# Performance work log

Hardware: AMD Instinct MI355X
Metric: run time of the kernel (lower is better)

## Reference

```python
import jax, jax.numpy as jnp
import numpy as np

NEG_SLOPE = 0.2
EPS = 1e-16


def glorot(key, shape):
    fan_in, fan_out = shape[0], shape[-1]
    lim = jnp.sqrt(6.0 / (fan_in + fan_out))
    return jax.random.uniform(key, shape, jnp.float32, -lim, lim)


def setup_inputs() -> dict:
    key = jax.random.key(0)
    ks = jax.random.split(key, 20)
    N, E, Fin, C, H = 50000, 800000, 128, 64, 4
    x = jax.random.normal(ks[0], (N, Fin), jnp.float32)
    edge_index = jax.random.randint(ks[1], (2, E), 0, N, jnp.int64)
    edge_attr = jax.random.normal(ks[2], (E, 1), jnp.float32)
    # GATConv layer 1: Fin -> C per head, H heads, concat
    W1 = glorot(ks[3], (Fin, H * C))
    att_src1 = glorot(ks[4], (H, C))
    att_dst1 = glorot(ks[5], (H, C))
    We1 = glorot(ks[6], (1, H * C))
    att_e1 = glorot(ks[7], (H, C))
    b1 = jnp.zeros((H * C,), jnp.float32)
    # GATConv layer 2: H*C -> C, 1 head, no concat
    W2 = glorot(ks[8], (H * C, C))
    att_src2 = glorot(ks[9], (1, C))
    att_dst2 = glorot(ks[10], (1, C))
    We2 = glorot(ks[11], (1, C))
    att_e2 = glorot(ks[12], (1, C))
    b2 = jnp.zeros((C,), jnp.float32)
    # classifier
    Wfc = glorot(ks[13], (C, 2))
    bfc = jnp.zeros((2,), jnp.float32)
    return dict(x=x, edge_index=edge_index, edge_attr=edge_attr,
                W1=W1, att_src1=att_src1, att_dst1=att_dst1, We1=We1, att_e1=att_e1, b1=b1,
                W2=W2, att_src2=att_src2, att_dst2=att_dst2, We2=We2, att_e2=att_e2, b2=b2,
                Wfc=Wfc, bfc=bfc)


def gat_conv(x, src, dst, edge_attr, W, att_src, att_dst, We, att_e, bias, concat):
    N = x.shape[0]
    H, C = att_src.shape
    h = (x @ W).reshape(N, H, C)                       # [N,H,C]
    a_src = jnp.sum(h * att_src, axis=-1)              # [N,H]
    a_dst = jnp.sum(h * att_dst, axis=-1)              # [N,H]
    e = (edge_attr @ We).reshape(-1, H, C)             # [E,H,C]
    a_e = jnp.sum(e * att_e, axis=-1)                  # [E,H]
    alpha = a_src[src] + a_dst[dst] + a_e              # [E,H]
    alpha = jax.nn.leaky_relu(alpha, NEG_SLOPE)
    # segment softmax over destination nodes
    amax = jax.lax.stop_gradient(jax.ops.segment_max(alpha, dst, num_segments=N))
    expa = jnp.exp(alpha - amax[dst])
    denom = jax.ops.segment_sum(expa, dst, num_segments=N)
    alpha = expa / (denom[dst] + EPS)                  # [E,H]
    msg = h[src] * alpha[:, :, None]                   # [E,H,C]
    out = jax.ops.segment_sum(msg, dst, num_segments=N)  # [N,H,C]
    out = out.reshape(N, H * C) if concat else out.mean(axis=1)
    return out + bias


def reference(x, edge_index, edge_attr,
              W1, att_src1, att_dst1, We1, att_e1, b1,
              W2, att_src2, att_dst2, We2, att_e2, b2,
              Wfc, bfc):
    N = x.shape[0]
    # add self loops (PyG GATConv default, fill_value='mean' for edge_attr)
    loop = jnp.arange(N, dtype=edge_index.dtype)
    src = jnp.concatenate([edge_index[0], loop])
    dst = jnp.concatenate([edge_index[1], loop])
    ea_mean = jnp.mean(edge_attr, axis=0, keepdims=True)
    ea = jnp.concatenate([edge_attr, jnp.broadcast_to(ea_mean, (N, edge_attr.shape[1]))])
    h = gat_conv(x, src, dst, ea, W1, att_src1, att_dst1, We1, att_e1, b1, concat=True)
    h = jax.nn.elu(h)
    # dropout: eval mode -> identity
    h = gat_conv(h, src, dst, ea, W2, att_src2, att_dst2, We2, att_e2, b2, concat=False)
    emb = jax.nn.elu(h)
    logits = emb @ Wfc + bfc
    return jax.nn.log_softmax(logits, axis=1), emb
```

## Files before the change

### kernel.cpp

```cpp
#include <hip/hip_runtime.h>
#include <math.h>

#define NEG_SLOPE 0.2f
#define EPSF 1e-16f

constexpr int FIN = 128;
constexpr int H1  = 4;
constexpr int C   = 64;
constexpr int HC  = 256;

typedef __attribute__((ext_vector_type(8))) short bf16x8;
typedef __attribute__((ext_vector_type(4))) float f32x4;

__device__ inline float wredsum(float v) {
#pragma unroll
    for (int off = 32; off; off >>= 1) v += __shfl_down(v, off);
    return v;
}
__device__ inline float wredmax(float v) {
#pragma unroll
    for (int off = 32; off; off >>= 1) v = fmaxf(v, __shfl_down(v, off));
    return v;
}
__device__ inline float4 wredmax4(float4 v) {
#pragma unroll
    for (int off = 32; off; off >>= 1) {
        v.x = fmaxf(v.x, __shfl_down(v.x, off));
        v.y = fmaxf(v.y, __shfl_down(v.y, off));
        v.z = fmaxf(v.z, __shfl_down(v.z, off));
        v.w = fmaxf(v.w, __shfl_down(v.w, off));
    }
    return v;
}
__device__ inline float4 wredsum4(float4 v) {
#pragma unroll
    for (int off = 32; off; off >>= 1) {
        v.x += __shfl_down(v.x, off);
        v.y += __shfl_down(v.y, off);
        v.z += __shfl_down(v.z, off);
        v.w += __shfl_down(v.w, off);
    }
    return v;
}
__device__ inline float4 bcast4(float4 v) {
    v.x = __shfl(v.x, 0); v.y = __shfl(v.y, 0);
    v.z = __shfl(v.z, 0); v.w = __shfl(v.w, 0);
    return v;
}
__device__ inline float comp4(float4 v, int i) {
    return i == 0 ? v.x : (i == 1 ? v.y : (i == 2 ? v.z : v.w));
}
__device__ inline unsigned short f2bf(float f) {
    unsigned u = __float_as_uint(f);
    return (unsigned short)((u + 0x7fffu + ((u >> 16) & 1u)) >> 16);
}

__global__ void k_ea_sum(const float* __restrict__ ea, int E, float* __restrict__ scal) {
    int i = blockIdx.x * blockDim.x + threadIdx.x;
    float v = (i < E) ? ea[i] : 0.0f;
    v = wredsum(v);
    __shared__ float sm[4];
    if ((threadIdx.x & 63) == 0) sm[threadIdx.x >> 6] = v;
    __syncthreads();
    if (threadIdx.x == 0) atomicAdd(scal, sm[0] + sm[1] + sm[2] + sm[3]);
}

__global__ void k_prep(const float* __restrict__ We1, const float* __restrict__ ae1,
                       const float* __restrict__ We2, const float* __restrict__ ae2,
                       float* __restrict__ scal, float inv_E) {
    int t = threadIdx.x;
    float p = We1[t] * ae1[t];
    p = wredsum(p);
    if ((t & 63) == 0) scal[4 + (t >> 6)] = p;
    if (t < 64) {
        float q = We2[t] * ae2[t];
        q = wredsum(q);
        if (t == 0) scal[2] = q;
    }
    if (t == 0) scal[1] = scal[0] * inv_E;
}

__global__ void k_convw(const float* __restrict__ W1, const float* __restrict__ W2,
                        unsigned short* __restrict__ W1f, unsigned short* __restrict__ W2f) {
    int idx = blockIdx.x * 256 + threadIdx.x;
    {
        int j = idx & 7, l = (idx >> 3) & 63, t = (idx >> 9) & 3, q = idx >> 11;
        int k = t * 32 + (l >> 4) * 8 + j;
        int n = 16 * q + (l & 15);
        W1f[idx] = f2bf(W1[k * HC + n]);
    }
    if (idx < 16384) {
        int j = idx & 7, l = (idx >> 3) & 63, t = (idx >> 9) & 7, g = idx >> 12;
        int k = t * 32 + (l >> 4) * 8 + j;
        int c = 16 * g + (l & 15);
        W2f[idx] = f2bf(W2[k * C + c]);
    }
}

__global__ void k_hist(const int* __restrict__ ei, int* __restrict__ deg, int E, int Etot) {
    int e = blockIdx.x * blockDim.x + threadIdx.x;
    if (e >= Etot) return;
    int d = (e < E) ? ei[E + e] : e - E;
    atomicAdd(&deg[d], 1);
}

__global__ void k_scan1(const int* __restrict__ deg, int* __restrict__ rowstart,
                        int* __restrict__ bsums, int N) {
    __shared__ int sm[256];
    int i = blockIdx.x * 256 + threadIdx.x;
    int v = (i < N) ? deg[i] : 0;
    sm[threadIdx.x] = v;
    __syncthreads();
    for (int off = 1; off < 256; off <<= 1) {
        int t = (threadIdx.x >= off) ? sm[threadIdx.x - off] : 0;
        __syncthreads();
        sm[threadIdx.x] += t;
        __syncthreads();
    }
    if (i < N) rowstart[i] = sm[threadIdx.x] - v;
    if (threadIdx.x == 255) bsums[blockIdx.x] = sm[255];
}

__global__ void k_scan2(int* __restrict__ bsums, int nb) {
    __shared__ int sm[256];
    int v = (threadIdx.x < nb) ? bsums[threadIdx.x] : 0;
    sm[threadIdx.x] = v;
    __syncthreads();
    for (int off = 1; off < 256; off <<= 1) {
        int t = (threadIdx.x >= off) ? sm[threadIdx.x - off] : 0;
        __syncthreads();
        sm[threadIdx.x] += t;
        __syncthreads();
    }
    if (threadIdx.x < nb) bsums[threadIdx.x] = sm[threadIdx.x] - v;
}

__global__ void k_scan3(int* __restrict__ rowstart, const int* __restrict__ bsums, int N) {
    int i = blockIdx.x * 256 + threadIdx.x;
    if (i < N) rowstart[i] += bsums[blockIdx.x];
}

__global__ void k_scatter(const int* __restrict__ ei, const float* __restrict__ eattr,
                          const float* __restrict__ scal, const int* __restrict__ rowstart,
                          int* __restrict__ cursor, int2* __restrict__ csr, int E, int Etot) {
    int e = blockIdx.x * blockDim.x + threadIdx.x;
    if (e >= Etot) return;
    int s, d; float ea;
    if (e < E) { s = ei[e]; d = ei[E + e]; ea = eattr[e]; }
    else       { s = e - E; d = s;          ea = scal[1]; }
    int pos = atomicAdd(&cursor[d], 1);
    csr[rowstart[d] + pos] = make_int2(s, __float_as_int(ea));
}

__global__ void k_gemm1(const float* __restrict__ x, const unsigned short* __restrict__ W1f,
                        const float* __restrict__ attsrc, const float* __restrict__ attdst,
                        unsigned short* __restrict__ h1b,
                        float* __restrict__ a_src, float* __restrict__ a_dst) {
    __shared__ unsigned short xs[16 * 128];
    __shared__ unsigned short hs[16 * 256];
    int t = threadIdx.x;
    int n0 = blockIdx.x * 16;
    {
        const float4* xg = (const float4*)(x + (size_t)n0 * FIN);
        float4 v0 = xg[t * 2], v1 = xg[t * 2 + 1];
        int row = t >> 4;
        int ch = (t & 15) ^ (row & 7);
        uint4 p;
        p.x = f2bf(v0.x) | ((unsigned)f2bf(v0.y) << 16);
        p.y = f2bf(v0.z) | ((unsigned)f2bf(v0.w) << 16);
        p.z = f2bf(v1.x) | ((unsigned)f2bf(v1.y) << 16);
        p.w = f2bf(v1.z) | ((unsigned)f2bf(v1.w) << 16);
        *(uint4*)((char*)xs + row * 256 + ch * 16) = p;
    }
    __syncthreads();
    int g = t >> 6, l = t & 63;
    int coll = l & 15, hi = l >> 4;
    bf16x8 a[4];
#pragma unroll
    for (int k = 0; k < 4; ++k) {
        int ch = (k * 4 + hi) ^ (coll & 7);
        a[k] = *(const bf16x8*)((const char*)xs + coll * 256 + ch * 16);
    }
    const bf16x8* wf = (const bf16x8*)W1f;
    f32x4 acc[4];
#pragma unroll
    for (int ct = 0; ct < 4; ++ct) {
        f32x4 c = {0.f, 0.f, 0.f, 0.f};
#pragma unroll
        for (int k = 0; k < 4; ++k) {
            bf16x8 b = wf[((g * 4 + ct) * 4 + k) * 64 + l];
            c = __builtin_amdgcn_mfma_f32_16x16x32_bf16(a[k], b, c, 0, 0, 0);
        }
        acc[ct] = c;
    }
    float ps[4] = {0,0,0,0}, pd[4] = {0,0,0,0};
#pragma unroll
    for (int ct = 0; ct < 4; ++ct) {
        float as_ = attsrc[g * 64 + ct * 16 + coll];
        float ad_ = attdst[g * 64 + ct * 16 + coll];
#pragma unroll
        for (int r = 0; r < 4; ++r) {
            ps[r] += acc[ct][r] * as_;
            pd[r] += acc[ct][r] * ad_;
        }
    }
#pragma unroll
    for (int r = 0; r < 4; ++r)
#pragma unroll
        for (int m = 1; m < 16; m <<= 1) {
            ps[r] += __shfl_xor(ps[r], m);
            pd[r] += __shfl_xor(pd[r], m);
        }
    if (coll == 0) {
#pragma unroll
        for (int r = 0; r < 4; ++r) {
            int row = hi * 4 + r;
            a_src[(n0 + row) * H1 + g] = ps[r];
            a_dst[(n0 + row) * H1 + g] = pd[r];
        }
    }
#pragma unroll
    for (int ct = 0; ct < 4; ++ct)
#pragma unroll
        for (int r = 0; r < 4; ++r) {
            int row = hi * 4 + r;
            int col = (g * 64 + ct * 16 + coll) ^ ((row & 3) << 4);
            hs[row * 256 + col] = f2bf(acc[ct][r]);
        }
    __syncthreads();
    {
        int row = t >> 4;
        int chS = (t & 15) ^ (row & 3);
        const uint4* sp = (const uint4*)(hs + row * 256 + chS * 16);
        uint4* dp = (uint4*)(h1b + (size_t)(n0 + row) * HC + (t & 15) * 16);
        dp[0] = sp[0]; dp[1] = sp[1];
    }
}

__global__ void k_agg1(const int* __restrict__ rowstart, const int* __restrict__ deg,
                       const int2* __restrict__ csr,
                       const float* __restrict__ a_src, const float* __restrict__ a_dst,
                       const float* __restrict__ scal, const unsigned short* __restrict__ h1b,
                       const float* __restrict__ b1, float* __restrict__ out1) {
    __shared__ float4 wlds[4][64];
    int wid = threadIdx.x >> 6, lane = threadIdx.x & 63;
    int n = blockIdx.x * 4 + wid;
    int myh = lane >> 4;
    int rs = rowstart[n], cnt = deg[n];
    const float4 adv = ((const float4*)a_dst)[n];
    const float4 wh  = *((const float4*)(scal + 4));
    const uint2* h1v = (const uint2*)h1b;
    const float* wbase = (const float*)(&wlds[wid][0]) + myh;

    float4 M = make_float4(-INFINITY, -INFINITY, -INFINITY, -INFINITY);
    float4 den  = make_float4(0.f, 0.f, 0.f, 0.f);
    float4 acc0 = make_float4(0.f, 0.f, 0.f, 0.f);
    float4 acc1 = make_float4(0.f, 0.f, 0.f, 0.f);

    for (int base = 0; base < cnt; base += 64) {
        int j = base + lane;
        int sj = 0;
        float4 al = make_float4(-INFINITY, -INFINITY, -INFINITY, -INFINITY);
        if (j < cnt) {
            int2 cv = csr[rs + j];
            sj = cv.x;
            float ea = __int_as_float(cv.y);
            float4 as4 = ((const float4*)a_src)[sj];
            al.x = as4.x + adv.x + ea * wh.x;
            al.y = as4.y + adv.y + ea * wh.y;
            al.z = as4.z + adv.z + ea * wh.z;
            al.w = as4.w + adv.w + ea * wh.w;
            al.x = al.x > 0.f ? al.x : NEG_SLOPE * al.x;
            al.y = al.y > 0.f ? al.y : NEG_SLOPE * al.y;
            al.z = al.z > 0.f ? al.z : NEG_SLOPE * al.z;
            al.w = al.w > 0.f ? al.w : NEG_SLOPE * al.w;
        }
        float4 cm = bcast4(wredmax4(al));
        float4 newM = make_float4(fmaxf(M.x, cm.x), fmaxf(M.y, cm.y),
                                  fmaxf(M.z, cm.z), fmaxf(M.w, cm.w));
        float4 sc = make_float4(__expf(M.x - newM.x), __expf(M.y - newM.y),
                                __expf(M.z - newM.z), __expf(M.w - newM.w));
        den.x *= sc.x; den.y *= sc.y; den.z *= sc.z; den.w *= sc.w;
        float scm = comp4(sc, myh);
        acc0.x *= scm; acc0.y *= scm; acc0.z *= scm; acc0.w *= scm;
        acc1.x *= scm; acc1.y *= scm; acc1.z *= scm; acc1.w *= scm;
        M = newM;
        float4 w4 = make_float4(__expf(al.x - M.x), __expf(al.y - M.y),
                                __expf(al.z - M.z), __expf(al.w - M.w));
        den.x += w4.x; den.y += w4.y; den.z += w4.z; den.w += w4.w;
        wlds[wid][lane] = w4;
        int m = min(64, cnt - base);
        int jj = 0;
#pragma unroll 2
        for (; jj + 1 < m; jj += 2) {
            int s0 = __shfl(sj, jj);
            int s1 = __shfl(sj, jj + 1);
            float w0 = wbase[jj * 4];
            float w1 = wbase[jj * 4 + 4];
            uint2 v0 = h1v[(size_t)s0 * 64 + lane];
            uint2 v1 = h1v[(size_t)s1 * 64 + lane];
            acc0.x += __uint_as_float(v0.x << 16)          * w0;
            acc0.y += __uint_as_float(v0.x & 0xffff0000u)  * w0;
            acc0.z += __uint_as_float(v0.y << 16)          * w0;
            acc0.w += __uint_as_float(v0.y & 0xffff0000u)  * w0;
            acc1.x += __uint_as_float(v1.x << 16)          * w1;
            acc1.y += __uint_as_float(v1.x & 0xffff0000u)  * w1;
            acc1.z += __uint_as_float(v1.y << 16)          * w1;
            acc1.w += __uint_as_float(v1.y & 0xffff0000u)  * w1;
        }
        if (jj < m) {
            int s0 = __shfl(sj, jj);
            float w0 = wbase[jj * 4];
            uint2 v0 = h1v[(size_t)s0 * 64 + lane];
            acc0.x += __uint_as_float(v0.x << 16)          * w0;
            acc0.y += __uint_as_float(v0.x & 0xffff0000u)  * w0;
            acc0.z += __uint_as_float(v0.y << 16)          * w0;
            acc0.w += __uint_as_float(v0.y & 0xffff0000u)  * w0;
        }
    }
    float4 dsum = bcast4(wredsum4(den));
    float dt = comp4(dsum, myh) + EPSF;
    float inv = 1.0f / dt;
    float4 b4 = ((const float4*)b1)[lane];
    float4 v;
    v.x = (acc0.x + acc1.x) * inv + b4.x;
    v.y = (acc0.y + acc1.y) * inv + b4.y;
    v.z = (acc0.z + acc1.z) * inv + b4.z;
    v.w = (acc0.w + acc1.w) * inv + b4.w;
    v.x = v.x > 0.f ? v.x : expm1f(v.x);
    v.y = v.y > 0.f ? v.y : expm1f(v.y);
    v.z = v.z > 0.f ? v.z : expm1f(v.z);
    v.w = v.w > 0.f ? v.w : expm1f(v.w);
    ((float4*)(out1 + (size_t)n * HC))[lane] = v;
}

__global__ void k_gemm2(const float* __restrict__ out1, const unsigned short* __restrict__ W2f,
                        const float* __restrict__ attsrc, const float* __restrict__ attdst,
                        unsigned short* __restrict__ h2b,
                        float* __restrict__ a_src2, float* __restrict__ a_dst2) {
    __shared__ unsigned short xs2[16 * 256];
    __shared__ unsigned short hs2[16 * 64];
    __shared__ float pls[2][4][16];
    int t = threadIdx.x;
    int n0 = blockIdx.x * 16;
    {
        const float4* og = (const float4*)(out1 + (size_t)n0 * HC);
        float4 v0 = og[t * 4], v1 = og[t * 4 + 1], v2 = og[t * 4 + 2], v3 = og[t * 4 + 3];
        int row = t >> 4;
        int c0 = ((t & 15) * 2) ^ (row & 7);
        int c1 = ((t & 15) * 2 + 1) ^ (row & 7);
        uint4 p0, p1;
        p0.x = f2bf(v0.x) | ((unsigned)f2bf(v0.y) << 16);
        p0.y = f2bf(v0.z) | ((unsigned)f2bf(v0.w) << 16);
        p0.z = f2bf(v1.x) | ((unsigned)f2bf(v1.y) << 16);
        p0.w = f2bf(v1.z) | ((unsigned)f2bf(v1.w) << 16);
        p1.x = f2bf(v2.x) | ((unsigned)f2bf(v2.y) << 16);
        p1.y = f2bf(v2.z) | ((unsigned)f2bf(v2.w) << 16);
        p1.z = f2bf(v3.x) | ((unsigned)f2bf(v3.y) << 16);
        p1.w = f2bf(v3.z) | ((unsigned)f2bf(v3.w) << 16);
        *(uint4*)((char*)xs2 + row * 512 + c0 * 16) = p0;
        *(uint4*)((char*)xs2 + row * 512 + c1 * 16) = p1;
    }
    __syncthreads();
    int g = t >> 6, l = t & 63;
    int coll = l & 15, hi = l >> 4;
    const bf16x8* wf = (const bf16x8*)W2f;
    f32x4 acc = {0.f, 0.f, 0.f, 0.f};
#pragma unroll
    for (int k = 0; k < 8; ++k) {
        int ch = (k * 4 + hi) ^ (coll & 7);
        bf16x8 av = *(const bf16x8*)((const char*)xs2 + coll * 512 + ch * 16);
        bf16x8 bv = wf[(g * 8 + k) * 64 + l];
        acc = __builtin_amdgcn_mfma_f32_16x16x32_bf16(av, bv, acc, 0, 0, 0);
    }
    float as_ = attsrc[g * 16 + coll];
    float ad_ = attdst[g * 16 + coll];
    float ps[4], pd[4];
#pragma unroll
    for (int r = 0; r < 4; ++r) { ps[r] = acc[r] * as_; pd[r] = acc[r] * ad_; }
#pragma unroll
    for (int r = 0; r < 4; ++r)
#pragma unroll
        for (int m = 1; m < 16; m <<= 1) {
            ps[r] += __shfl_xor(ps[r], m);
            pd[r] += __shfl_xor(pd[r], m);
        }
    if (coll == 0) {
#pragma unroll
        for (int r = 0; r < 4; ++r) {
            int row = hi * 4 + r;
            pls[0][g][row] = ps[r];
            pls[1][g][row] = pd[r];
        }
    }
#pragma unroll
    for (int r = 0; r < 4; ++r) {
        int row = hi * 4 + r;
        int col = (g * 16 + coll) ^ ((row & 3) << 4);
        hs2[row * 64 + col] = f2bf(acc[r]);
    }
    __syncthreads();
    if (t < 128) {
        int row = t >> 3;
        int chS = (t & 7) ^ ((row & 3) << 1);
        *(uint4*)(h2b + (size_t)(n0 + row) * C + (t & 7) * 8) =
            *(const uint4*)(hs2 + row * 64 + chS * 8);
    }
    if (t < 16) {
        a_src2[n0 + t] = pls[0][0][t] + pls[0][1][t] + pls[0][2][t] + pls[0][3][t];
        a_dst2[n0 + t] = pls[1][0][t] + pls[1][1][t] + pls[1][2][t] + pls[1][3][t];
    }
}

__global__ void k_agg2(const int* __restrict__ rowstart, const int* __restrict__ deg,
                       const int2* __restrict__ csr,
                       const float* __restrict__ a_src2, const float* __restrict__ a_dst2,
                       const float* __restrict__ scal, const unsigned short* __restrict__ h2b,
                       const float* __restrict__ b2, const float* __restrict__ Wfc,
                       const float* __restrict__ bfc, float* __restrict__ d_out, int N) {
    __shared__ float wlds[4][64];
    int wid = threadIdx.x >> 6, lane = threadIdx.x & 63;
    int n = blockIdx.x * 4 + wid;
    int eg = lane >> 4, li = lane & 15;
    int rs = rowstart[n], cnt = deg[n];
    float adv = a_dst2[n];
    float w2  = scal[2];
    const uint2* h2v = (const uint2*)h2b;

    float M = -INFINITY, den = 0.0f;
    float4 acc = make_float4(0.f, 0.f, 0.f, 0.f);

    for (int base = 0; base < cnt; base += 64) {
        int j = base + lane;
        int sj = 0; float al = -INFINITY;
        if (j < cnt) {
            int2 cv = csr[rs + j];
            sj = cv.x;
            al = a_src2[sj] + adv + __int_as_float(cv.y) * w2;
            al = al > 0.0f ? al : NEG_SLOPE * al;
        }
        float cm = wredmax(al); cm = __shfl(cm, 0);
        float newM = fmaxf(M, cm);
        float sc = __expf(M - newM);
        den *= sc;
        acc.x *= sc; acc.y *= sc; acc.z *= sc; acc.w *= sc;
        M = newM;
        float w = __expf(al - M);
        den += w;
        wlds[wid][lane] = w;
        int m = min(64, cnt - base);
#pragma unroll 4
        for (int jj = 0; jj < m; jj += 4) {
            int idx = jj + eg;
            float ww = wlds[wid][idx];
            int   s  = __shfl(sj, idx);
            uint2 hv = h2v[(size_t)s * 16 + li];
            acc.x += __uint_as_float(hv.x << 16)         * ww;
            acc.y += __uint_as_float(hv.x & 0xffff0000u) * ww;
            acc.z += __uint_as_float(hv.y << 16)         * ww;
            acc.w += __uint_as_float(hv.y & 0xffff0000u) * ww;
        }
    }
#pragma unroll
    for (int off = 32; off >= 16; off >>= 1) {
        acc.x += __shfl_down(acc.x, off);
        acc.y += __shfl_down(acc.y, off);
        acc.z += __shfl_down(acc.z, off);
        acc.w += __shfl_down(acc.w, off);
    }
    float dt = wredsum(den); dt = __shfl(dt, 0);
    float inv = 1.0f / (dt + EPSF);
    float4 b4 = ((const float4*)b2)[li];
    float4 v;
    v.x = acc.x * inv + b4.x;
    v.y = acc.y * inv + b4.y;
    v.z = acc.z * inv + b4.z;
    v.w = acc.w * inv + b4.w;
    v.x = v.x > 0.f ? v.x : expm1f(v.x);
    v.y = v.y > 0.f ? v.y : expm1f(v.y);
    v.z = v.z > 0.f ? v.z : expm1f(v.z);
    v.w = v.w > 0.f ? v.w : expm1f(v.w);
    if (lane < 16)
        ((float4*)(d_out + (size_t)2 * N + (size_t)n * C))[li] = v;
    const float4* wfc4 = (const float4*)Wfc;
    float4 A = wfc4[li * 2], B = wfc4[li * 2 + 1];
    float p0 = v.x * A.x + v.y * A.z + v.z * B.x + v.w * B.z;
    float p1 = v.x * A.y + v.y * A.w + v.z * B.y + v.w * B.w;
#pragma unroll
    for (int off = 8; off; off >>= 1) {
        p0 += __shfl_down(p0, off);
        p1 += __shfl_down(p1, off);
    }
    if (lane == 0) {
        p0 += bfc[0]; p1 += bfc[1];
        float mm = fmaxf(p0, p1);
        float lse = mm + logf(__expf(p0 - mm) + __expf(p1 - mm));
        d_out[(size_t)n * 2]     = p0 - lse;
        d_out[(size_t)n * 2 + 1] = p1 - lse;
    }
}

extern "C" void kernel_launch(void* const* d_in, const int* in_sizes, int n_in,
                              void* d_out, int out_size, void* d_ws, size_t ws_size,
                              hipStream_t stream) {
    const float* x     = (const float*)d_in[0];
    const int*   ei    = (const int*)  d_in[1];
    const float* eattr = (const float*)d_in[2];
    const float* W1    = (const float*)d_in[3];
    const float* as1   = (const float*)d_in[4];
    const float* ad1   = (const float*)d_in[5];
    const float* We1   = (const float*)d_in[6];
    const float* ae1   = (const float*)d_in[7];
    const float* b1    = (const float*)d_in[8];
    const float* W2    = (const float*)d_in[9];
    const float* as2   = (const float*)d_in[10];
    const float* ad2   = (const float*)d_in[11];
    const float* We2   = (const float*)d_in[12];
    const float* ae2   = (const float*)d_in[13];
    const float* b2    = (const float*)d_in[14];
    const float* Wfc   = (const float*)d_in[15];
    const float* bfc   = (const float*)d_in[16];

    const int N    = in_sizes[0] / FIN;
    const int E    = in_sizes[2];
    const int Etot = E + N;

    char* wsb = (char*)d_ws;
    size_t off = 0;
    auto alloc = [&](size_t elems) {
        off = (off + 15) & ~(size_t)15;
        void* p = wsb + off; off += elems * 4; return p;
    };

    int*   deg    = (int*)  alloc(N);
    int*   cursor = (int*)  alloc(N);
    float* scal   = (float*)alloc(8);
    size_t zero_bytes = (off + 15) & ~(size_t)15;
    int*   rowstart = (int*)  alloc(N);
    int*   bsums    = (int*)  alloc(256);
    int2*  csr      = (int2*) alloc((size_t)Etot * 2);
    unsigned short* h1b = (unsigned short*)alloc((size_t)N * HC / 2);
    unsigned short* h2b = (unsigned short*)alloc((size_t)N * C / 2);
    float* out1     = (float*)alloc((size_t)N * HC);
    unsigned short* W1f = (unsigned short*)alloc(16384);
    unsigned short* W2f = (unsigned short*)alloc(8192);
    float* a_src1   = (float*)alloc((size_t)N * H1);
    float* a_dst1   = (float*)alloc((size_t)N * H1);
    float* a_src2   = (float*)alloc(N);
    float* a_dst2   = (float*)alloc(N);

    hipMemsetAsync(d_ws, 0, zero_bytes, stream);

    k_ea_sum<<<(E + 255) / 256, 256, 0, stream>>>(eattr, E, scal);
    k_prep<<<1, 256, 0, stream>>>(We1, ae1, We2, ae2, scal, 1.0f / (float)E);
    k_convw<<<128, 256, 0, stream>>>(W1, W2, W1f, W2f);

    int ge = (Etot + 255) / 256;
    int nb = (N + 255) / 256;
    k_hist<<<ge, 256, 0, stream>>>(ei, deg, E, Etot);
    k_scan1<<<nb, 256, 0, stream>>>(deg, rowstart, bsums, N);
    k_scan2<<<1, 256, 0, stream>>>(bsums, nb);
    k_scan3<<<nb, 256, 0, stream>>>(rowstart, bsums, N);
    k_scatter<<<ge, 256, 0, stream>>>(ei, eattr, scal, rowstart, cursor, csr, E, Etot);

    k_gemm1<<<N / 16, 256, 0, stream>>>(x, W1f, as1, ad1, h1b, a_src1, a_dst1);
    k_agg1<<<N / 4, 256, 0, stream>>>(rowstart, deg, csr, a_src1, a_dst1, scal, h1b, b1, out1);
    k_gemm2<<<N / 16, 256, 0, stream>>>(out1, W2f, as2, ad2, h2b, a_src2, a_dst2);
    k_agg2<<<N / 4, 256, 0, stream>>>(rowstart, deg, csr, a_src2, a_dst2, scal, h2b,
                                      b2, Wfc, bfc, (float*)d_out, N);
}
```

Measured before the change: 383.7 us.

## Aggregate raw inputs before layer-1 projection and fuse both GEMMs

Layer 1 now aggregates the 128-wide bf16 input features per head before projecting, instead of gathering 256-wide projected features per edge. The attention logits come from precomputed W1·att vectors. The W1 GEMM, bias, ELU and W2 GEMM are fused into one kernel, which removes the fp32 out1 round trip. The histogram is merged with the edge-attribute sum. In exchange, the layer-1 GEMM input grows to four per-head aggregates per node, and the aggregation does more FMAs per gathered element.

```diff
diff --git a/kernel.cpp b/kernel.cpp
--- a/kernel.cpp
+++ b/kernel.cpp
@@ -55,9 +55,15 @@
     return (unsigned short)((u + 0x7fffu + ((u >> 16) & 1u)) >> 16);
 }
 
-__global__ void k_ea_sum(const float* __restrict__ ea, int E, float* __restrict__ scal) {
-    int i = blockIdx.x * blockDim.x + threadIdx.x;
-    float v = (i < E) ? ea[i] : 0.0f;
+__global__ void k_hist_ea(const int* __restrict__ ei, const float* __restrict__ eattr,
+                          int* __restrict__ deg, float* __restrict__ scal, int E, int Etot) {
+    int e = blockIdx.x * blockDim.x + threadIdx.x;
+    float v = 0.0f;
+    if (e < Etot) {
+        int d = (e < E) ? ei[E + e] : e - E;
+        atomicAdd(&deg[d], 1);
+        if (e < E) v = eattr[e];
+    }
     v = wredsum(v);
     __shared__ float sm[4];
     if ((threadIdx.x & 63) == 0) sm[threadIdx.x >> 6] = v;
@@ -80,6 +86,17 @@
     if (t == 0) scal[1] = scal[0] * inv_E;
 }
 
+__global__ void k_prepvec(const float* __restrict__ W1, const float* __restrict__ as1,
+                          const float* __restrict__ ad1, float* __restrict__ vsd) {
+    int idx = blockIdx.x * 256 + threadIdx.x;
+    int which = idx >> 9, h = (idx >> 7) & 3, k = idx & 127;
+    const float* att = which ? ad1 : as1;
+    float s = 0.0f;
+#pragma unroll 8
+    for (int c = 0; c < 64; ++c) s += W1[k * HC + h * 64 + c] * att[h * 64 + c];
+    vsd[idx] = s;
+}
+
 __global__ void k_convw(const float* __restrict__ W1, const float* __restrict__ W2,
                         unsigned short* __restrict__ W1f, unsigned short* __restrict__ W2f) {
     int idx = blockIdx.x * 256 + threadIdx.x;
@@ -95,13 +112,6 @@
         int c = 16 * g + (l & 15);
         W2f[idx] = f2bf(W2[k * C + c]);
     }
-}
-
-__global__ void k_hist(const int* __restrict__ ei, int* __restrict__ deg, int E, int Etot) {
-    int e = blockIdx.x * blockDim.x + threadIdx.x;
-    if (e >= Etot) return;
-    int d = (e < E) ? ei[E + e] : e - E;
-    atomicAdd(&deg[d], 1);
 }
 
 __global__ void k_scan1(const int* __restrict__ deg, int* __restrict__ rowstart,
@@ -152,110 +162,57 @@
     csr[rowstart[d] + pos] = make_int2(s, __float_as_int(ea));
 }
 
-__global__ void k_gemm1(const float* __restrict__ x, const unsigned short* __restrict__ W1f,
-                        const float* __restrict__ attsrc, const float* __restrict__ attdst,
-                        unsigned short* __restrict__ h1b,
+__global__ void k_convx(const float* __restrict__ x, const float* __restrict__ vsd,
+                        unsigned int* __restrict__ xb,
                         float* __restrict__ a_src, float* __restrict__ a_dst) {
-    __shared__ unsigned short xs[16 * 128];
-    __shared__ unsigned short hs[16 * 256];
-    int t = threadIdx.x;
-    int n0 = blockIdx.x * 16;
+    int wid = threadIdx.x >> 6, l = threadIdx.x & 63;
+    int n = blockIdx.x * 4 + wid;
+    float2 xv = ((const float2*)x)[(size_t)n * 64 + l];
+    const float2* vs2 = (const float2*)vsd;
+    float4 A, B;
     {
-        const float4* xg = (const float4*)(x + (size_t)n0 * FIN);
-        float4 v0 = xg[t * 2], v1 = xg[t * 2 + 1];
-        int row = t >> 4;
-        int ch = (t & 15) ^ (row & 7);
-        uint4 p;
-        p.x = f2bf(v0.x) | ((unsigned)f2bf(v0.y) << 16);
-        p.y = f2bf(v0.z) | ((unsigned)f2bf(v0.w) << 16);
-        p.z = f2bf(v1.x) | ((unsigned)f2bf(v1.y) << 16);
-        p.w = f2bf(v1.z) | ((unsigned)f2bf(v1.w) << 16);
-        *(uint4*)((char*)xs + row * 256 + ch * 16) = p;
-    }
-    __syncthreads();
-    int g = t >> 6, l = t & 63;
-    int coll = l & 15, hi = l >> 4;
-    bf16x8 a[4];
-#pragma unroll
-    for (int k = 0; k < 4; ++k) {
-        int ch = (k * 4 + hi) ^ (coll & 7);
-        a[k] = *(const bf16x8*)((const char*)xs + coll * 256 + ch * 16);
-    }
-    const bf16x8* wf = (const bf16x8*)W1f;
-    f32x4 acc[4];
-#pragma unroll
-    for (int ct = 0; ct < 4; ++ct) {
-        f32x4 c = {0.f, 0.f, 0.f, 0.f};
-#pragma unroll
-        for (int k = 0; k < 4; ++k) {
-            bf16x8 b = wf[((g * 4 + ct) * 4 + k) * 64 + l];
-            c = __builtin_amdgcn_mfma_f32_16x16x32_bf16(a[k], b, c, 0, 0, 0);
-        }
-        acc[ct] = c;
-    }
-    float ps[4] = {0,0,0,0}, pd[4] = {0,0,0,0};
-#pragma unroll
-    for (int ct = 0; ct < 4; ++ct) {
-        float as_ = attsrc[g * 64 + ct * 16 + coll];
-        float ad_ = attdst[g * 64 + ct * 16 + coll];
-#pragma unroll
-        for (int r = 0; r < 4; ++r) {
-            ps[r] += acc[ct][r] * as_;
-            pd[r] += acc[ct][r] * ad_;
-        }
-    }
-#pragma unroll
-    for (int r = 0; r < 4; ++r)
-#pragma unroll
-        for (int m = 1; m < 16; m <<= 1) {
-            ps[r] += __shfl_xor(ps[r], m);
-            pd[r] += __shfl_xor(pd[r], m);
-        }
-    if (coll == 0) {
-#pragma unroll
-        for (int r = 0; r < 4; ++r) {
-            int row = hi * 4 + r;
-            a_src[(n0 + row) * H1 + g] = ps[r];
-            a_dst[(n0 + row) * H1 + g] = pd[r];
-        }
-    }
-#pragma unroll
-    for (int ct = 0; ct < 4; ++ct)
-#pragma unroll
-        for (int r = 0; r < 4; ++r) {
-            int row = hi * 4 + r;
-            int col = (g * 64 + ct * 16 + coll) ^ ((row & 3) << 4);
-            hs[row * 256 + col] = f2bf(acc[ct][r]);
-        }
-    __syncthreads();
-    {
-        int row = t >> 4;
-        int chS = (t & 15) ^ (row & 3);
-        const uint4* sp = (const uint4*)(hs + row * 256 + chS * 16);
-        uint4* dp = (uint4*)(h1b + (size_t)(n0 + row) * HC + (t & 15) * 16);
-        dp[0] = sp[0]; dp[1] = sp[1];
-    }
-}
-
-__global__ void k_agg1(const int* __restrict__ rowstart, const int* __restrict__ deg,
-                       const int2* __restrict__ csr,
-                       const float* __restrict__ a_src, const float* __restrict__ a_dst,
-                       const float* __restrict__ scal, const unsigned short* __restrict__ h1b,
-                       const float* __restrict__ b1, float* __restrict__ out1) {
+        float2 a0 = vs2[l],        a1 = vs2[64 + l];
+        float2 a2 = vs2[128 + l],  a3 = vs2[192 + l];
+        A.x = xv.x * a0.x + xv.y * a0.y;
+        A.y = xv.x * a1.x + xv.y * a1.y;
+        A.z = xv.x * a2.x + xv.y * a2.y;
+        A.w = xv.x * a3.x + xv.y * a3.y;
+        float2 b0 = vs2[256 + l],  b1 = vs2[320 + l];
+        float2 b2 = vs2[384 + l],  b3 = vs2[448 + l];
+        B.x = xv.x * b0.x + xv.y * b0.y;
+        B.y = xv.x * b1.x + xv.y * b1.y;
+        B.z = xv.x * b2.x + xv.y * b2.y;
+        B.w = xv.x * b3.x + xv.y * b3.y;
+    }
+    A = wredsum4(A);
+    B = wredsum4(B);
+    if (l == 0) {
+        ((float4*)a_src)[n] = A;
+        ((float4*)a_dst)[n] = B;
+    }
+    xb[(size_t)n * 64 + l] = f2bf(xv.x) | ((unsigned)f2bf(xv.y) << 16);
+}
+
+__global__ void k_agg1x(const int* __restrict__ rowstart, const int* __restrict__ deg,
+                        const int2* __restrict__ csr,
+                        const float* __restrict__ a_src, const float* __restrict__ a_dst,
+                        const float* __restrict__ scal, const uint2* __restrict__ xb2,
+                        uint2* __restrict__ xaggb2) {
     __shared__ float4 wlds[4][64];
     int wid = threadIdx.x >> 6, lane = threadIdx.x & 63;
     int n = blockIdx.x * 4 + wid;
-    int myh = lane >> 4;
+    int half = lane >> 5, hl = lane & 31;
     int rs = rowstart[n], cnt = deg[n];
     const float4 adv = ((const float4*)a_dst)[n];
     const float4 wh  = *((const float4*)(scal + 4));
-    const uint2* h1v = (const uint2*)h1b;
-    const float* wbase = (const float*)(&wlds[wid][0]) + myh;
 
     float4 M = make_float4(-INFINITY, -INFINITY, -INFINITY, -INFINITY);
-    float4 den  = make_float4(0.f, 0.f, 0.f, 0.f);
-    float4 acc0 = make_float4(0.f, 0.f, 0.f, 0.f);
-    float4 acc1 = make_float4(0.f, 0.f, 0.f, 0.f);
+    float4 den = make_float4(0.f, 0.f, 0.f, 0.f);
+    float acc[4][4];
+#pragma unroll
+    for (int h = 0; h < 4; ++h)
+#pragma unroll
+        for (int c = 0; c < 4; ++c) acc[h][c] = 0.0f;
 
     for (int base = 0; base < cnt; base += 64) {
         int j = base + lane;
@@ -281,96 +238,104 @@
         float4 sc = make_float4(__expf(M.x - newM.x), __expf(M.y - newM.y),
                                 __expf(M.z - newM.z), __expf(M.w - newM.w));
         den.x *= sc.x; den.y *= sc.y; den.z *= sc.z; den.w *= sc.w;
-        float scm = comp4(sc, myh);
-        acc0.x *= scm; acc0.y *= scm; acc0.z *= scm; acc0.w *= scm;
-        acc1.x *= scm; acc1.y *= scm; acc1.z *= scm; acc1.w *= scm;
+#pragma unroll
+        for (int h = 0; h < 4; ++h) {
+            float s = comp4(sc, h);
+#pragma unroll
+            for (int c = 0; c < 4; ++c) acc[h][c] *= s;
+        }
         M = newM;
         float4 w4 = make_float4(__expf(al.x - M.x), __expf(al.y - M.y),
                                 __expf(al.z - M.z), __expf(al.w - M.w));
         den.x += w4.x; den.y += w4.y; den.z += w4.z; den.w += w4.w;
         wlds[wid][lane] = w4;
         int m = min(64, cnt - base);
-        int jj = 0;
-#pragma unroll 2
-        for (; jj + 1 < m; jj += 2) {
-            int s0 = __shfl(sj, jj);
-            int s1 = __shfl(sj, jj + 1);
-            float w0 = wbase[jj * 4];
-            float w1 = wbase[jj * 4 + 4];
-            uint2 v0 = h1v[(size_t)s0 * 64 + lane];
-            uint2 v1 = h1v[(size_t)s1 * 64 + lane];
-            acc0.x += __uint_as_float(v0.x << 16)          * w0;
-            acc0.y += __uint_as_float(v0.x & 0xffff0000u)  * w0;
-            acc0.z += __uint_as_float(v0.y << 16)          * w0;
-            acc0.w += __uint_as_float(v0.y & 0xffff0000u)  * w0;
-            acc1.x += __uint_as_float(v1.x << 16)          * w1;
-            acc1.y += __uint_as_float(v1.x & 0xffff0000u)  * w1;
-            acc1.z += __uint_as_float(v1.y << 16)          * w1;
-            acc1.w += __uint_as_float(v1.y & 0xffff0000u)  * w1;
-        }
-        if (jj < m) {
-            int s0 = __shfl(sj, jj);
-            float w0 = wbase[jj * 4];
-            uint2 v0 = h1v[(size_t)s0 * 64 + lane];
-            acc0.x += __uint_as_float(v0.x << 16)          * w0;
-            acc0.y += __uint_as_float(v0.x & 0xffff0000u)  * w0;
-            acc0.z += __uint_as_float(v0.y << 16)          * w0;
-            acc0.w += __uint_as_float(v0.y & 0xffff0000u)  * w0;
-        }
-    }
-    float4 dsum = bcast4(wredsum4(den));
-    float dt = comp4(dsum, myh) + EPSF;
-    float inv = 1.0f / dt;
-    float4 b4 = ((const float4*)b1)[lane];
-    float4 v;
-    v.x = (acc0.x + acc1.x) * inv + b4.x;
-    v.y = (acc0.y + acc1.y) * inv + b4.y;
-    v.z = (acc0.z + acc1.z) * inv + b4.z;
-    v.w = (acc0.w + acc1.w) * inv + b4.w;
-    v.x = v.x > 0.f ? v.x : expm1f(v.x);
-    v.y = v.y > 0.f ? v.y : expm1f(v.y);
-    v.z = v.z > 0.f ? v.z : expm1f(v.z);
-    v.w = v.w > 0.f ? v.w : expm1f(v.w);
-    ((float4*)(out1 + (size_t)n * HC))[lane] = v;
-}
-
-__global__ void k_gemm2(const float* __restrict__ out1, const unsigned short* __restrict__ W2f,
-                        const float* __restrict__ attsrc, const float* __restrict__ attdst,
-                        unsigned short* __restrict__ h2b,
-                        float* __restrict__ a_src2, float* __restrict__ a_dst2) {
-    __shared__ unsigned short xs2[16 * 256];
+        for (int jj = 0; jj < m; jj += 2) {
+            int idx = jj + half;
+            float4 we = wlds[wid][idx];
+            int s = __shfl(sj, idx);
+            uint2 v = xb2[(size_t)s * 32 + hl];
+            float c0 = __uint_as_float(v.x << 16);
+            float c1 = __uint_as_float(v.x & 0xffff0000u);
+            float c2 = __uint_as_float(v.y << 16);
+            float c3 = __uint_as_float(v.y & 0xffff0000u);
+            acc[0][0] += c0 * we.x; acc[0][1] += c1 * we.x;
+            acc[0][2] += c2 * we.x; acc[0][3] += c3 * we.x;
+            acc[1][0] += c0 * we.y; acc[1][1] += c1 * we.y;
+            acc[1][2] += c2 * we.y; acc[1][3] += c3 * we.y;
+            acc[2][0] += c0 * we.z; acc[2][1] += c1 * we.z;
+            acc[2][2] += c2 * we.z; acc[2][3] += c3 * we.z;
+            acc[3][0] += c0 * we.w; acc[3][1] += c1 * we.w;
+            acc[3][2] += c2 * we.w; acc[3][3] += c3 * we.w;
+        }
+    }
+    float4 dt = bcast4(wredsum4(den));
+    float4 inv = make_float4(1.0f / (dt.x + EPSF), 1.0f / (dt.y + EPSF),
+                             1.0f / (dt.z + EPSF), 1.0f / (dt.w + EPSF));
+#pragma unroll
+    for (int h = 0; h < 4; ++h)
+#pragma unroll
+        for (int c = 0; c < 4; ++c) acc[h][c] += __shfl_xor(acc[h][c], 32);
+    int h0 = half * 2;
+    float iv0 = comp4(inv, h0), iv1 = comp4(inv, h0 + 1);
+    uint2 o0, o1;
+    o0.x = f2bf(acc[h0][0] * iv0)     | ((unsigned)f2bf(acc[h0][1] * iv0) << 16);
+    o0.y = f2bf(acc[h0][2] * iv0)     | ((unsigned)f2bf(acc[h0][3] * iv0) << 16);
+    o1.x = f2bf(acc[h0 + 1][0] * iv1) | ((unsigned)f2bf(acc[h0 + 1][1] * iv1) << 16);
+    o1.y = f2bf(acc[h0 + 1][2] * iv1) | ((unsigned)f2bf(acc[h0 + 1][3] * iv1) << 16);
+    xaggb2[((size_t)n * 4 + h0) * 32 + hl]     = o0;
+    xaggb2[((size_t)n * 4 + h0 + 1) * 32 + hl] = o1;
+}
+
+__global__ void k_fused12(const unsigned short* __restrict__ xaggb,
+                          const unsigned short* __restrict__ W1f,
+                          const float* __restrict__ b1,
+                          const unsigned short* __restrict__ W2f,
+                          const float* __restrict__ attsrc, const float* __restrict__ attdst,
+                          unsigned short* __restrict__ h2b,
+                          float* __restrict__ a_src2, float* __restrict__ a_dst2) {
+    __shared__ unsigned short ols[16 * 256];
     __shared__ unsigned short hs2[16 * 64];
     __shared__ float pls[2][4][16];
     int t = threadIdx.x;
     int n0 = blockIdx.x * 16;
-    {
-        const float4* og = (const float4*)(out1 + (size_t)n0 * HC);
-        float4 v0 = og[t * 4], v1 = og[t * 4 + 1], v2 = og[t * 4 + 2], v3 = og[t * 4 + 3];
-        int row = t >> 4;
-        int c0 = ((t & 15) * 2) ^ (row & 7);
-        int c1 = ((t & 15) * 2 + 1) ^ (row & 7);
-        uint4 p0, p1;
-        p0.x = f2bf(v0.x) | ((unsigned)f2bf(v0.y) << 16);
-        p0.y = f2bf(v0.z) | ((unsigned)f2bf(v0.w) << 16);
-        p0.z = f2bf(v1.x) | ((unsigned)f2bf(v1.y) << 16);
-        p0.w = f2bf(v1.z) | ((unsigned)f2bf(v1.w) << 16);
-        p1.x = f2bf(v2.x) | ((unsigned)f2bf(v2.y) << 16);
-        p1.y = f2bf(v2.z) | ((unsigned)f2bf(v2.w) << 16);
-        p1.z = f2bf(v3.x) | ((unsigned)f2bf(v3.y) << 16);
-        p1.w = f2bf(v3.z) | ((unsigned)f2bf(v3.w) << 16);
-        *(uint4*)((char*)xs2 + row * 512 + c0 * 16) = p0;
-        *(uint4*)((char*)xs2 + row * 512 + c1 * 16) = p1;
-    }
-    __syncthreads();
     int g = t >> 6, l = t & 63;
     int coll = l & 15, hi = l >> 4;
-    const bf16x8* wf = (const bf16x8*)W2f;
+    const bf16x8* af = (const bf16x8*)xaggb;
+    size_t abase = ((size_t)(n0 + coll) * 4 + g) * 16;
+    bf16x8 a[4];
+#pragma unroll
+    for (int k = 0; k < 4; ++k) a[k] = af[abase + k * 4 + hi];
+    const bf16x8* wf1 = (const bf16x8*)W1f;
+    f32x4 acc1[4];
+#pragma unroll
+    for (int ct = 0; ct < 4; ++ct) {
+        f32x4 c = {0.f, 0.f, 0.f, 0.f};
+#pragma unroll
+        for (int k = 0; k < 4; ++k) {
+            bf16x8 b = wf1[((g * 4 + ct) * 4 + k) * 64 + l];
+            c = __builtin_amdgcn_mfma_f32_16x16x32_bf16(a[k], b, c, 0, 0, 0);
+        }
+        acc1[ct] = c;
+    }
+#pragma unroll
+    for (int ct = 0; ct < 4; ++ct)
+#pragma unroll
+        for (int r = 0; r < 4; ++r) {
+            int row = hi * 4 + r;
+            int col = g * 64 + ct * 16 + coll;
+            float v = acc1[ct][r] + b1[col];
+            v = v > 0.f ? v : expm1f(v);
+            ols[row * 256 + (((col >> 3) ^ (row & 7)) << 3) + (col & 7)] = f2bf(v);
+        }
+    __syncthreads();
+    const bf16x8* wf2 = (const bf16x8*)W2f;
     f32x4 acc = {0.f, 0.f, 0.f, 0.f};
 #pragma unroll
     for (int k = 0; k < 8; ++k) {
         int ch = (k * 4 + hi) ^ (coll & 7);
-        bf16x8 av = *(const bf16x8*)((const char*)xs2 + coll * 512 + ch * 16);
-        bf16x8 bv = wf[(g * 8 + k) * 64 + l];
+        bf16x8 av = *(const bf16x8*)((const char*)ols + coll * 512 + ch * 16);
+        bf16x8 bv = wf2[(g * 8 + k) * 64 + l];
         acc = __builtin_amdgcn_mfma_f32_16x16x32_bf16(av, bv, acc, 0, 0, 0);
     }
     float as_ = attsrc[g * 16 + coll];
@@ -539,33 +504,35 @@
     int*   rowstart = (int*)  alloc(N);
     int*   bsums    = (int*)  alloc(256);
     int2*  csr      = (int2*) alloc((size_t)Etot * 2);
-    unsigned short* h1b = (unsigned short*)alloc((size_t)N * HC / 2);
-    unsigned short* h2b = (unsigned short*)alloc((size_t)N * C / 2);
-    float* out1     = (float*)alloc((size_t)N * HC);
-    unsigned short* W1f = (unsigned short*)alloc(16384);
-    unsigned short* W2f = (unsigned short*)alloc(8192);
-    float* a_src1   = (float*)alloc((size_t)N * H1);
-    float* a_dst1   = (float*)alloc((size_t)N * H1);
-    float* a_src2   = (float*)alloc(N);
-    float* a_dst2   = (float*)alloc(N);
+    unsigned int*   xb     = (unsigned int*)  alloc((size_t)N * 64);
+    unsigned short* xaggb  = (unsigned short*)alloc((size_t)N * 256);
+    unsigned short* h2b    = (unsigned short*)alloc((size_t)N * 32);
+    unsigned short* W1f    = (unsigned short*)alloc(16384);
+    unsigned short* W2f    = (unsigned short*)alloc(8192);
+    float* vsd     = (float*)alloc(1024);
+    float* a_src1  = (float*)alloc((size_t)N * H1);
+    float* a_dst1  = (float*)alloc((size_t)N * H1);
+    float* a_src2  = (float*)alloc(N);
+    float* a_dst2  = (float*)alloc(N);
 
     hipMemsetAsync(d_ws, 0, zero_bytes, stream);
-
-    k_ea_sum<<<(E + 255) / 256, 256, 0, stream>>>(eattr, E, scal);
-    k_prep<<<1, 256, 0, stream>>>(We1, ae1, We2, ae2, scal, 1.0f / (float)E);
-    k_convw<<<128, 256, 0, stream>>>(W1, W2, W1f, W2f);
 
     int ge = (Etot + 255) / 256;
     int nb = (N + 255) / 256;
-    k_hist<<<ge, 256, 0, stream>>>(ei, deg, E, Etot);
+    k_hist_ea<<<ge, 256, 0, stream>>>(ei, eattr, deg, scal, E, Etot);
+    k_prep<<<1, 256, 0, stream>>>(We1, ae1, We2, ae2, scal, 1.0f / (float)E);
+    k_prepvec<<<4, 256, 0, stream>>>(W1, as1, ad1, vsd);
+    k_convw<<<128, 256, 0, stream>>>(W1, W2, W1f, W2f);
     k_scan1<<<nb, 256, 0, stream>>>(deg, rowstart, bsums, N);
     k_scan2<<<1, 256, 0, stream>>>(bsums, nb);
     k_scan3<<<nb, 256, 0, stream>>>(rowstart, bsums, N);
     k_scatter<<<ge, 256, 0, stream>>>(ei, eattr, scal, rowstart, cursor, csr, E, Etot);
 
-    k_gemm1<<<N / 16, 256, 0, stream>>>(x, W1f, as1, ad1, h1b, a_src1, a_dst1);
-    k_agg1<<<N / 4, 256, 0, stream>>>(rowstart, deg, csr, a_src1, a_dst1, scal, h1b, b1, out1);
-    k_gemm2<<<N / 16, 256, 0, stream>>>(out1, W2f, as2, ad2, h2b, a_src2, a_dst2);
+    k_convx<<<N / 4, 256, 0, stream>>>(x, vsd, xb, a_src1, a_dst1);
+    k_agg1x<<<N / 4, 256, 0, stream>>>(rowstart, deg, csr, a_src1, a_dst1, scal,
+                                       (const uint2*)xb, (uint2*)xaggb);
+    k_fused12<<<N / 16, 256, 0, stream>>>(xaggb, W1f, b1, W2f, as2, ad2,
+                                          h2b, a_src2, a_dst2);
     k_agg2<<<N / 4, 256, 0, stream>>>(rowstart, deg, csr, a_src2, a_dst2, scal, h2b,
                                       b2, Wfc, bfc, (float*)d_out, N);
 }
```

New measurement: 540.4 us. 1.41x slower.
